# Optimization experiments

Hardware: AMD Instinct MI355X
Metric: run time of the kernel (lower is better)

## Reference

```python
import jax, jax.numpy as jnp
import numpy as np

P = 50000    # number of POIs (rows of HG_pu, size of square A)
U = 100000   # number of users (rows of HG_up)
NNZ = 1600000
D = 128      # emb_dim


def setup_inputs() -> dict:
    key = jax.random.key(0)
    ks = jax.random.split(key, 8)
    x = jax.random.normal(ks[0], (P, D), dtype=jnp.float32)
    e = jax.random.normal(ks[1], (P, D), dtype=jnp.float32)
    vals_up = jax.random.uniform(ks[2], (NNZ,), dtype=jnp.float32)
    vals_pu = jax.random.uniform(ks[3], (NNZ,), dtype=jnp.float32)
    rows_up = jax.random.randint(ks[4], (NNZ,), 0, U, dtype=jnp.int32)
    cols_up = jax.random.randint(ks[5], (NNZ,), 0, P, dtype=jnp.int32)
    rows_pu = jax.random.randint(ks[6], (NNZ,), 0, P, dtype=jnp.int32)
    cols_pu = jax.random.randint(ks[7], (NNZ,), 0, U, dtype=jnp.int32)
    return {"t": 0, "x": x, "e": e,
            "vals_up": vals_up, "vals_pu": vals_pu,
            "rows_up": rows_up, "cols_up": cols_up,
            "rows_pu": rows_pu, "cols_pu": cols_pu}


def _spmm(vals, rows, cols, dense, num_rows):
    # sparse [num_rows, *] @ dense -> [num_rows, D]
    gathered = vals[:, None] * dense[cols]          # [nnz, D]
    return jax.ops.segment_sum(gathered, rows, num_segments=num_rows)


def reference(t, x, e, vals_up, vals_pu, rows_up, cols_up, rows_pu, cols_pu):
    # A = HG_pu @ HG_up (never materialized);  out = (A - I) @ x + e
    y = _spmm(vals_up, rows_up, cols_up, x, U)      # HG_up @ x : [U, D]
    z = _spmm(vals_pu, rows_pu, cols_pu, y, P)      # HG_pu @ y : [P, D]
    return z - x + e                                # (A - I) x + e
```

## Files before the change

### kernel.cpp

```cpp
#include <hip/hip_runtime.h>

#define NP 50000
#define NU 100000
#define NNZ_C 1600000
#define NNZ2 (2 * NNZ_C)
#define DIM 128
#define NR_TOT (NU + NP)

#define RBSH 7
#define RB 128
#define NBK ((NR_TOT + RB - 1) / RB)
#define ITEMS 8192
#define NBLK ((NNZ2 + ITEMS - 1) / ITEMS)
#define CHUNK 4096
#define CPT (CHUNK / 256)

__device__ inline unsigned pack_bf16x2(float a, float b) {
    unsigned ia = __float_as_uint(a), ib = __float_as_uint(b);
    ia = (ia + 0x7FFFu + ((ia >> 16) & 1u)) >> 16;
    ib = (ib + 0x7FFFu + ((ib >> 16) & 1u)) >> 16;
    return ia | (ib << 16);
}

__device__ inline float dec_val(unsigned p) {
    return __uint_as_float((p & 0x7FFFu) << 16);
}

__global__ void cvt_bf16_kernel(const float* __restrict__ x,
                                unsigned* __restrict__ xh, int nwords) {
    int i = blockIdx.x * blockDim.x + threadIdx.x;
    if (i >= nwords) return;
    float2 v = ((const float2*)x)[i];
    xh[i] = pack_bf16x2(v.x, v.y);
}


__global__ void p1_hist_kernel(const int* __restrict__ rows_up,
                               const int* __restrict__ rows_pu,
                               int* __restrict__ hist_all) {
    __shared__ int h[NBK];
    for (int k = threadIdx.x; k < NBK; k += 256) h[k] = 0;
    __syncthreads();
    int base = blockIdx.x * ITEMS;
    for (int k = 0; k < ITEMS / 256; ++k) {
        int i = base + k * 256 + threadIdx.x;
        if (i >= NNZ2) break;
        int r = (i < NNZ_C) ? rows_up[i] : (NU + rows_pu[i - NNZ_C]);
        atomicAdd(&h[r >> RBSH], 1);
    }
    __syncthreads();
    for (int k = threadIdx.x; k < NBK; k += 256)
        hist_all[k * NBLK + blockIdx.x] = h[k];
}

__global__ void p1_scan_kernel(const int* __restrict__ hist_all,
                               int* __restrict__ base_all,
                               int* __restrict__ totals) {
    __shared__ int lds[512];
    int b = blockIdx.x;
    int v = (threadIdx.x < NBLK) ? hist_all[b * NBLK + threadIdx.x] : 0;
    lds[threadIdx.x] = v;
    __syncthreads();
    for (int off = 1; off < 512; off <<= 1) {
        int t = (threadIdx.x >= (unsigned)off) ? lds[threadIdx.x - off] : 0;
        __syncthreads();
        lds[threadIdx.x] += t;
        __syncthreads();
    }
    if (threadIdx.x < NBLK) base_all[b * NBLK + threadIdx.x] = lds[threadIdx.x] - v;
    if (threadIdx.x == 511) totals[b] = lds[511];
}

__global__ void bucket_base_scan_kernel(const int* __restrict__ totals,
                                        int* __restrict__ bbase) {
    __shared__ int lds[1024];
    __shared__ int carry;
    if (threadIdx.x == 0) carry = 0;
    __syncthreads();
    for (int start = 0; start < NBK; start += 1024) {
        int i = start + threadIdx.x;
        int v = (i < NBK) ? totals[i] : 0;
        lds[threadIdx.x] = v;
        __syncthreads();
        for (int off = 1; off < 1024; off <<= 1) {
            int t = (threadIdx.x >= (unsigned)off) ? lds[threadIdx.x - off] : 0;
            __syncthreads();
            lds[threadIdx.x] += t;
            __syncthreads();
        }
        if (i < NBK) bbase[i] = carry + lds[threadIdx.x] - v;
        int tot = lds[1023];
        __syncthreads();
        if (threadIdx.x == 0) carry += tot;
        __syncthreads();
    }
    if (threadIdx.x == 0) bbase[NBK] = carry;
}

__global__ void p1_scatter_kernel(const float* __restrict__ vals_up,
                                  const float* __restrict__ vals_pu,
                                  const int* __restrict__ rows_up,
                                  const int* __restrict__ rows_pu,
                                  const int* __restrict__ cols_up,
                                  const int* __restrict__ cols_pu,
                                  const int* __restrict__ base_all,
                                  const int* __restrict__ bbase,
                                  unsigned* __restrict__ stag_pay,
                                  unsigned char* __restrict__ stag_row) {
    __shared__ unsigned spay[CHUNK];
    __shared__ unsigned char srow[CHUNK];
    __shared__ int sdst[CHUNK];
    __shared__ int h[NBK];
    __shared__ int cbase[NBK];
    __shared__ int off[NBK];
    __shared__ int tsum[256];

    int tid = threadIdx.x;
    int blk = blockIdx.x;
    for (int k = tid; k < NBK; k += 256)
        cbase[k] = bbase[k] + base_all[k * NBLK + blk];
    int base = blk * ITEMS;

    for (int c = 0; c < ITEMS / CHUNK; ++c) {
        int cbeg = base + c * CHUNK;
        int cnt_items = NNZ2 - cbeg;
        if (cnt_items <= 0) break;
        if (cnt_items > CHUNK) cnt_items = CHUNK;

        for (int k = tid; k < NBK; k += 256) { h[k] = 0; off[k] = 0; }
        __syncthreads();

        unsigned rpay[CPT];
        int rrow[CPT];
        for (int k = 0; k < CPT; ++k) {
            int i = cbeg + k * 256 + tid;
            if (i < NNZ2) {
                int r, cc; float v;
                if (i < NNZ_C) { r = rows_up[i]; cc = cols_up[i]; v = vals_up[i]; }
                else { int q = i - NNZ_C; r = NU + rows_pu[q]; cc = cols_pu[q]; v = vals_pu[q]; }
                unsigned vb = __float_as_uint(v);
                unsigned vr = (vb + 0x7FFFu + ((vb >> 16) & 1u)) >> 16;
                rpay[k] = ((unsigned)cc << 15) | vr;
                rrow[k] = r;
                atomicAdd(&h[r >> RBSH], 1);
            } else {
                rrow[k] = -1;
            }
        }
        __syncthreads();

        {
            int s0 = tid * 5;
            int s1 = s0 + 5; if (s1 > NBK) s1 = NBK; if (s0 > NBK) s0 = NBK;
            int a = 0;
            for (int s = s0; s < s1; ++s) a += h[s];
            tsum[tid] = a;
            __syncthreads();
            for (int o = 1; o < 256; o <<= 1) {
                int t2 = (tid >= o) ? tsum[tid - o] : 0;
                __syncthreads();
                tsum[tid] += t2;
                __syncthreads();
            }
            int run = (tid == 0) ? 0 : tsum[tid - 1];
            for (int s = s0; s < s1; ++s) { int cc2 = h[s]; h[s] = run; run += cc2; }
        }
        __syncthreads();

        for (int k = 0; k < CPT; ++k) {
            if (rrow[k] < 0) continue;
            int b = rrow[k] >> RBSH;
            int lp = atomicAdd(&off[b], 1);
            int slot = h[b] + lp;
            spay[slot] = rpay[k];
            srow[slot] = (unsigned char)(rrow[k] & (RB - 1));
            sdst[slot] = cbase[b] + lp;
        }
        __syncthreads();

        for (int s = tid; s < cnt_items; s += 256) {
            int d = sdst[s];
            stag_pay[d] = spay[s];
            stag_row[d] = srow[s];
        }
        __syncthreads();
        for (int k = tid; k < NBK; k += 256) cbase[k] += off[k];
        __syncthreads();
    }
}

__global__ void p2_finalize_kernel(const unsigned* __restrict__ stag_pay,
                                   const unsigned char* __restrict__ stag_row,
                                   const int* __restrict__ bbase,
                                   unsigned* __restrict__ packed,
                                   int* __restrict__ row_beg,
                                   int* __restrict__ row_cnt) {
    __shared__ int cnt[RB];
    __shared__ int scn[RB];
    __shared__ int cur[RB];
    int b = blockIdx.x;
    int beg = bbase[b], end = bbase[b + 1];
    if (threadIdx.x < RB) cnt[threadIdx.x] = 0;
    __syncthreads();
    for (int i = beg + threadIdx.x; i < end; i += 256)
        atomicAdd(&cnt[stag_row[i]], 1);
    __syncthreads();
    if (threadIdx.x < RB) scn[threadIdx.x] = cnt[threadIdx.x];
    __syncthreads();
    for (int off = 1; off < RB; off <<= 1) {
        int t = 0;
        if (threadIdx.x < RB && threadIdx.x >= (unsigned)off) t = scn[threadIdx.x - off];
        __syncthreads();
        if (threadIdx.x < RB) scn[threadIdx.x] += t;
        __syncthreads();
    }
    if (threadIdx.x < RB) {
        int excl = scn[threadIdx.x] - cnt[threadIdx.x];
        cur[threadIdx.x] = beg + excl;
        int rr = (b << RBSH) + threadIdx.x;
        if (rr < NR_TOT) { row_beg[rr] = beg + excl; row_cnt[rr] = cnt[threadIdx.x]; }
    }
    __syncthreads();
    for (int i = beg + threadIdx.x; i < end; i += 256) {
        int pos = atomicAdd(&cur[stag_row[i]], 1);
        packed[pos] = stag_pay[i];
    }
}


#define NZ_FMA(P, U)                                            \
    do {                                                         \
        acc.x += dec_val(P) * __uint_as_float((U) << 16);        \
        acc.y += dec_val(P) * __uint_as_float((U) & 0xFFFF0000u);\
    } while (0)

__device__ inline void gather_row(const unsigned* __restrict__ packed,
                                  const unsigned* __restrict__ src,
                                  int beg, int end, int lane, float2& acc) {
    beg = __builtin_amdgcn_readfirstlane(beg);
    end = __builtin_amdgcn_readfirstlane(end);
    int n = end - beg;
    const unsigned* prow = packed + beg;
    int j = 0;
    for (; j + 8 <= n; j += 8) {
        unsigned p0 = prow[j + 0];
        unsigned p1 = prow[j + 1];
        unsigned p2 = prow[j + 2];
        unsigned p3 = prow[j + 3];
        unsigned p4 = prow[j + 4];
        unsigned p5 = prow[j + 5];
        unsigned p6 = prow[j + 6];
        unsigned p7 = prow[j + 7];
        unsigned u0 = src[(p0 >> 15) * 64 + lane];
        unsigned u1 = src[(p1 >> 15) * 64 + lane];
        unsigned u2 = src[(p2 >> 15) * 64 + lane];
        unsigned u3 = src[(p3 >> 15) * 64 + lane];
        unsigned u4 = src[(p4 >> 15) * 64 + lane];
        unsigned u5 = src[(p5 >> 15) * 64 + lane];
        unsigned u6 = src[(p6 >> 15) * 64 + lane];
        unsigned u7 = src[(p7 >> 15) * 64 + lane];
        NZ_FMA(p0, u0); NZ_FMA(p1, u1); NZ_FMA(p2, u2); NZ_FMA(p3, u3);
        NZ_FMA(p4, u4); NZ_FMA(p5, u5); NZ_FMA(p6, u6); NZ_FMA(p7, u7);
    }
    for (; j + 4 <= n; j += 4) {
        unsigned p0 = prow[j + 0];
        unsigned p1 = prow[j + 1];
        unsigned p2 = prow[j + 2];
        unsigned p3 = prow[j + 3];
        unsigned u0 = src[(p0 >> 15) * 64 + lane];
        unsigned u1 = src[(p1 >> 15) * 64 + lane];
        unsigned u2 = src[(p2 >> 15) * 64 + lane];
        unsigned u3 = src[(p3 >> 15) * 64 + lane];
        NZ_FMA(p0, u0); NZ_FMA(p1, u1); NZ_FMA(p2, u2); NZ_FMA(p3, u3);
    }
    for (; j < n; ++j) {
        unsigned p = prow[j];
        unsigned u = src[(p >> 15) * 64 + lane];
        NZ_FMA(p, u);
    }
}

__global__ void spmm_gather_kernel(const int* __restrict__ row_beg,
                                   const int* __restrict__ row_cnt,
                                   const unsigned* __restrict__ packed,
                                   const unsigned* __restrict__ src,
                                   unsigned* __restrict__ dst) {
    int r = blockIdx.x * 4 + (threadIdx.x >> 6);
    if (r >= NU) return;
    int lane = threadIdx.x & 63;
    int beg = row_beg[r], end = beg + row_cnt[r];
    float2 acc = make_float2(0.f, 0.f);
    gather_row(packed, src, beg, end, lane, acc);
    dst[r * 64 + lane] = pack_bf16x2(acc.x, acc.y);
}

__global__ void spmm_gather_fused_kernel(const int* __restrict__ row_beg,
                                         const int* __restrict__ row_cnt,
                                         const unsigned* __restrict__ packed,
                                         const unsigned* __restrict__ src,
                                         const float* __restrict__ x,
                                         const float* __restrict__ e,
                                         float* __restrict__ out) {
    int r = blockIdx.x * 4 + (threadIdx.x >> 6);
    if (r >= NP) return;
    int lane = threadIdx.x & 63;
    int beg = row_beg[NU + r], end = beg + row_cnt[NU + r];
    float2 acc = make_float2(0.f, 0.f);
    gather_row(packed, src, beg, end, lane, acc);
    float2 xv = ((const float2*)(x + (size_t)r * DIM))[lane];
    float2 ev = ((const float2*)(e + (size_t)r * DIM))[lane];
    float2 o;
    o.x = acc.x - xv.x + ev.x;
    o.y = acc.y - xv.y + ev.y;
    ((float2*)(out + (size_t)r * DIM))[lane] = o;
}

extern "C" void kernel_launch(void* const* d_in, const int* in_sizes, int n_in,
                              void* d_out, int out_size, void* d_ws, size_t ws_size,
                              hipStream_t stream) {
    const float* x       = (const float*)d_in[1];
    const float* e       = (const float*)d_in[2];
    const float* vals_up = (const float*)d_in[3];
    const float* vals_pu = (const float*)d_in[4];
    const int*   rows_up = (const int*)d_in[5];
    const int*   cols_up = (const int*)d_in[6];
    const int*   rows_pu = (const int*)d_in[7];
    const int*   cols_pu = (const int*)d_in[8];
    float* out = (float*)d_out;

    char* ws = (char*)d_ws;
    unsigned* yh          = (unsigned*)(ws);
    unsigned* stag_pay    = (unsigned*)(ws);
    unsigned char* stag_row = (unsigned char*)(ws + 12800000);
    unsigned* xh     = (unsigned*)(ws + 25600000);
    unsigned* packed = (unsigned*)(ws + 38400000);
    int* hist_all    = (int*)(ws + 51200000);
    int* base_all    = (int*)(ws + 53033248);
    int* totals      = (int*)(ws + 54866496);
    int* bbase       = (int*)(ws + 54871184);
    int* row_beg     = (int*)(ws + 54875904);
    int* row_cnt     = (int*)(ws + 55475904);

    cvt_bf16_kernel<<<(NP * 64 + 255) / 256, 256, 0, stream>>>(x, xh, NP * 64);

    p1_hist_kernel<<<NBLK, 256, 0, stream>>>(rows_up, rows_pu, hist_all);
    p1_scan_kernel<<<NBK, 512, 0, stream>>>(hist_all, base_all, totals);
    bucket_base_scan_kernel<<<1, 1024, 0, stream>>>(totals, bbase);
    p1_scatter_kernel<<<NBLK, 256, 0, stream>>>(vals_up, vals_pu,
                                                rows_up, rows_pu,
                                                cols_up, cols_pu,
                                                base_all, bbase,
                                                stag_pay, stag_row);
    p2_finalize_kernel<<<NBK, 256, 0, stream>>>(stag_pay, stag_row, bbase,
                                                packed, row_beg, row_cnt);

    spmm_gather_kernel<<<(NU + 3) / 4, 256, 0, stream>>>(row_beg, row_cnt,
                                                         packed, xh, yh);

    spmm_gather_fused_kernel<<<(NP + 3) / 4, 256, 0, stream>>>(row_beg, row_cnt,
                                                               packed, yh,
                                                               x, e, out);
}
```

Before: 348.3 us.

## Halve scatter block size to one chunk per block and compact LDS staging

Cuts the items per scatter block to a single chunk, doubling the number of blocks. The per-chunk loop and its extra barriers go away and more blocks can run in parallel. The histogram scan now handles two entries per thread to cover the doubled block count. The separate row-byte and destination arrays in shared memory become one packed bucket/row word, and each destination is recomputed from the bucket base plus the slot offset. hist_all and base_all move into the packed region of the workspace, which is not yet written when they are used. In exchange, hist_all and base_all double in size and more blocks each load cbase.

```diff
diff --git a/kernel.cpp b/kernel.cpp
--- a/kernel.cpp
+++ b/kernel.cpp
@@ -10,7 +10,7 @@
 #define RBSH 7
 #define RB 128
 #define NBK ((NR_TOT + RB - 1) / RB)
-#define ITEMS 8192
+#define ITEMS 4096
 #define NBLK ((NNZ2 + ITEMS - 1) / ITEMS)
 #define CHUNK 4096
 #define CPT (CHUNK / 256)
@@ -58,8 +58,11 @@
                                int* __restrict__ totals) {
     __shared__ int lds[512];
     int b = blockIdx.x;
-    int v = (threadIdx.x < NBLK) ? hist_all[b * NBLK + threadIdx.x] : 0;
-    lds[threadIdx.x] = v;
+    int t0 = threadIdx.x * 2;
+    int e0 = (t0 < NBLK) ? hist_all[b * NBLK + t0] : 0;
+    int e1 = (t0 + 1 < NBLK) ? hist_all[b * NBLK + t0 + 1] : 0;
+    int a = e0 + e1;
+    lds[threadIdx.x] = a;
     __syncthreads();
     for (int off = 1; off < 512; off <<= 1) {
         int t = (threadIdx.x >= (unsigned)off) ? lds[threadIdx.x - off] : 0;
@@ -67,7 +70,9 @@
         lds[threadIdx.x] += t;
         __syncthreads();
     }
-    if (threadIdx.x < NBLK) base_all[b * NBLK + threadIdx.x] = lds[threadIdx.x] - v;
+    int excl = lds[threadIdx.x] - a;
+    if (t0 < NBLK) base_all[b * NBLK + t0] = excl;
+    if (t0 + 1 < NBLK) base_all[b * NBLK + t0 + 1] = excl + e0;
     if (threadIdx.x == 511) totals[b] = lds[511];
 }
 
@@ -108,8 +113,7 @@
                                   unsigned* __restrict__ stag_pay,
                                   unsigned char* __restrict__ stag_row) {
     __shared__ unsigned spay[CHUNK];
-    __shared__ unsigned char srow[CHUNK];
-    __shared__ int sdst[CHUNK];
+    __shared__ unsigned sbr[CHUNK];
     __shared__ int h[NBK];
     __shared__ int cbase[NBK];
     __shared__ int off[NBK];
@@ -117,75 +121,70 @@
 
     int tid = threadIdx.x;
     int blk = blockIdx.x;
-    for (int k = tid; k < NBK; k += 256)
+    for (int k = tid; k < NBK; k += 256) {
         cbase[k] = bbase[k] + base_all[k * NBLK + blk];
-    int base = blk * ITEMS;
-
-    for (int c = 0; c < ITEMS / CHUNK; ++c) {
-        int cbeg = base + c * CHUNK;
-        int cnt_items = NNZ2 - cbeg;
-        if (cnt_items <= 0) break;
-        if (cnt_items > CHUNK) cnt_items = CHUNK;
-
-        for (int k = tid; k < NBK; k += 256) { h[k] = 0; off[k] = 0; }
-        __syncthreads();
-
-        unsigned rpay[CPT];
-        int rrow[CPT];
-        for (int k = 0; k < CPT; ++k) {
-            int i = cbeg + k * 256 + tid;
-            if (i < NNZ2) {
-                int r, cc; float v;
-                if (i < NNZ_C) { r = rows_up[i]; cc = cols_up[i]; v = vals_up[i]; }
-                else { int q = i - NNZ_C; r = NU + rows_pu[q]; cc = cols_pu[q]; v = vals_pu[q]; }
-                unsigned vb = __float_as_uint(v);
-                unsigned vr = (vb + 0x7FFFu + ((vb >> 16) & 1u)) >> 16;
-                rpay[k] = ((unsigned)cc << 15) | vr;
-                rrow[k] = r;
-                atomicAdd(&h[r >> RBSH], 1);
-            } else {
-                rrow[k] = -1;
-            }
+        h[k] = 0;
+        off[k] = 0;
+    }
+    __syncthreads();
+
+    int cbeg = blk * ITEMS;
+    int cnt_items = NNZ2 - cbeg;
+    if (cnt_items > CHUNK) cnt_items = CHUNK;
+
+    unsigned rpay[CPT];
+    int rrow[CPT];
+    for (int k = 0; k < CPT; ++k) {
+        int i = cbeg + k * 256 + tid;
+        if (i < NNZ2) {
+            int r, cc; float v;
+            if (i < NNZ_C) { r = rows_up[i]; cc = cols_up[i]; v = vals_up[i]; }
+            else { int q = i - NNZ_C; r = NU + rows_pu[q]; cc = cols_pu[q]; v = vals_pu[q]; }
+            unsigned vb = __float_as_uint(v);
+            unsigned vr = (vb + 0x7FFFu + ((vb >> 16) & 1u)) >> 16;
+            rpay[k] = ((unsigned)cc << 15) | vr;
+            rrow[k] = r;
+            atomicAdd(&h[r >> RBSH], 1);
+        } else {
+            rrow[k] = -1;
         }
-        __syncthreads();
-
-        {
-            int s0 = tid * 5;
-            int s1 = s0 + 5; if (s1 > NBK) s1 = NBK; if (s0 > NBK) s0 = NBK;
-            int a = 0;
-            for (int s = s0; s < s1; ++s) a += h[s];
-            tsum[tid] = a;
+    }
+    __syncthreads();
+
+    {
+        int s0 = tid * 5;
+        int s1 = s0 + 5; if (s1 > NBK) s1 = NBK; if (s0 > NBK) s0 = NBK;
+        int a = 0;
+        for (int s = s0; s < s1; ++s) a += h[s];
+        tsum[tid] = a;
+        __syncthreads();
+        for (int o = 1; o < 256; o <<= 1) {
+            int t2 = (tid >= o) ? tsum[tid - o] : 0;
             __syncthreads();
-            for (int o = 1; o < 256; o <<= 1) {
-                int t2 = (tid >= o) ? tsum[tid - o] : 0;
-                __syncthreads();
-                tsum[tid] += t2;
-                __syncthreads();
-            }
-            int run = (tid == 0) ? 0 : tsum[tid - 1];
-            for (int s = s0; s < s1; ++s) { int cc2 = h[s]; h[s] = run; run += cc2; }
+            tsum[tid] += t2;
+            __syncthreads();
         }
-        __syncthreads();
-
-        for (int k = 0; k < CPT; ++k) {
-            if (rrow[k] < 0) continue;
-            int b = rrow[k] >> RBSH;
-            int lp = atomicAdd(&off[b], 1);
-            int slot = h[b] + lp;
-            spay[slot] = rpay[k];
-            srow[slot] = (unsigned char)(rrow[k] & (RB - 1));
-            sdst[slot] = cbase[b] + lp;
-        }
-        __syncthreads();
-
-        for (int s = tid; s < cnt_items; s += 256) {
-            int d = sdst[s];
-            stag_pay[d] = spay[s];
-            stag_row[d] = srow[s];
-        }
-        __syncthreads();
-        for (int k = tid; k < NBK; k += 256) cbase[k] += off[k];
-        __syncthreads();
+        int run = (tid == 0) ? 0 : tsum[tid - 1];
+        for (int s = s0; s < s1; ++s) { int cc2 = h[s]; h[s] = run; run += cc2; }
+    }
+    __syncthreads();
+
+    for (int k = 0; k < CPT; ++k) {
+        if (rrow[k] < 0) continue;
+        int b = rrow[k] >> RBSH;
+        int lp = atomicAdd(&off[b], 1);
+        int slot = h[b] + lp;
+        spay[slot] = rpay[k];
+        sbr[slot] = ((unsigned)b << 8) | (unsigned)(rrow[k] & (RB - 1));
+    }
+    __syncthreads();
+
+    for (int s = tid; s < cnt_items; s += 256) {
+        unsigned br = sbr[s];
+        int b = (int)(br >> 8);
+        int d = cbase[b] + (s - h[b]);
+        stag_pay[d] = spay[s];
+        stag_row[d] = (unsigned char)(br & 255u);
     }
 }
 
@@ -334,8 +333,8 @@
     unsigned char* stag_row = (unsigned char*)(ws + 12800000);
     unsigned* xh     = (unsigned*)(ws + 25600000);
     unsigned* packed = (unsigned*)(ws + 38400000);
-    int* hist_all    = (int*)(ws + 51200000);
-    int* base_all    = (int*)(ws + 53033248);
+    int* hist_all    = (int*)(ws + 38400000);
+    int* base_all    = (int*)(ws + 42065216);
     int* totals      = (int*)(ws + 54866496);
     int* bbase       = (int*)(ws + 54871184);
     int* row_beg     = (int*)(ws + 54875904);
```

After: 336.2 us. -3.5%, faster.
